# Performance work log

Hardware: AMD Instinct MI355X
Metric: run time of the kernel (lower is better)

Reference implementation:

```python
import jax, jax.numpy as jnp
import numpy as np

C_S, C_Z, N_HEADS = 768, 64, 12
HEAD_DIM = C_S // N_HEADS
L = 1024
EPS = 1e-5


def _ln(x, g, b):
    mu = jnp.mean(x, axis=-1, keepdims=True)
    var = jnp.mean((x - mu) ** 2, axis=-1, keepdims=True)
    return (x - mu) * jax.lax.rsqrt(var + EPS) * g + b


def setup_inputs() -> dict:
    key = jax.random.key(0)
    ks = jax.random.split(key, 12)
    w = lambda k, shp, fan_in: jax.random.normal(k, shp, dtype=jnp.float32) / np.sqrt(fan_in)
    return {
        "single": jax.random.normal(ks[0], (L, C_S), dtype=jnp.float32),
        "pair": jax.random.normal(ks[1], (L, L, C_Z), dtype=jnp.float32),
        "ln_s_g": jnp.ones((C_S,), jnp.float32),
        "ln_s_b": jnp.zeros((C_S,), jnp.float32),
        "ln_z_g": jnp.ones((C_Z,), jnp.float32),
        "ln_z_b": jnp.zeros((C_Z,), jnp.float32),
        "Wq": w(ks[2], (C_S, C_S), C_S),
        "Wk": w(ks[3], (C_S, C_S), C_S),
        "Wv": w(ks[4], (C_S, C_S), C_S),
        "Wb": w(ks[5], (C_Z, N_HEADS), C_Z),
        "Wout": w(ks[6], (C_S, C_S), C_S),
        "bout": jnp.zeros((C_S,), jnp.float32),
        "Wgate": w(ks[7], (C_S, C_S), C_S),
        "bgate": jnp.zeros((C_S,), jnp.float32),
    }


def reference(single, pair, ln_s_g, ln_s_b, ln_z_g, ln_z_b,
              Wq, Wk, Wv, Wb, Wout, bout, Wgate, bgate):
    Lq = single.shape[0]
    s = _ln(single, ln_s_g, ln_s_b)                    # [L, C_S]
    z = _ln(pair, ln_z_g, ln_z_b)                      # [L, L, C_Z]
    q = (s @ Wq).reshape(Lq, N_HEADS, HEAD_DIM)
    k = (s @ Wk).reshape(Lq, N_HEADS, HEAD_DIM)
    v = (s @ Wv).reshape(Lq, N_HEADS, HEAD_DIM)
    logits = jnp.einsum('ihd,jhd->hij', q, k) / np.sqrt(HEAD_DIM)
    logits = logits + jnp.einsum('ijc,ch->hij', z, Wb)  # pair bias per head
    attn = jax.nn.softmax(logits, axis=-1)              # [H, L, L]
    out = jnp.einsum('hij,jhd->ihd', attn, v).reshape(Lq, C_S)
    return single + jax.nn.sigmoid(s @ Wgate + bgate) * (out @ Wout + bout)
```

## Files before the change

kernel.cpp:

```cpp
#include <hip/hip_runtime.h>

#define LQ 1024
#define CS 768
#define CZ 64
#define NH 12
#define HD 64

typedef float4 f4;
using bf16x8 = __attribute__((ext_vector_type(8))) short;
using f32x4  = __attribute__((ext_vector_type(4))) float;

static __device__ __forceinline__ unsigned short f2bf(float f) {
  unsigned int u = __float_as_uint(f);
  u += 0x7fffu + ((u >> 16) & 1u);
  return (unsigned short)(u >> 16);
}
static __device__ __forceinline__ float bf2f(unsigned short b) {
  return __uint_as_float(((unsigned int)b) << 16);
}
static __device__ __forceinline__ unsigned cvtpk(float lo, float hi) {
  unsigned r;
  asm("v_cvt_pk_bf16_f32 %0, %1, %2" : "=v"(r) : "v"(lo), "v"(hi));
  return r;
}

__global__ __launch_bounds__(256) void ln_wconv_k(
    const float* __restrict__ x, const float* __restrict__ g,
    const float* __restrict__ b, unsigned short* __restrict__ s_out,
    const float* __restrict__ Wq, const float* __restrict__ Wk,
    const float* __restrict__ Wv, const float* __restrict__ Wg,
    const float* __restrict__ Wo, unsigned short* __restrict__ wt) {
  const int bid = blockIdx.x;
  const int t = threadIdx.x;
  if (bid < LQ) {
    const int row = bid;
    const float* xr = x + (size_t)row * CS;
    float v0 = xr[t], v1 = xr[t + 256], v2 = xr[t + 512];
    float s1 = v0 + v1 + v2;
    float s2 = v0 * v0 + v1 * v1 + v2 * v2;
#pragma unroll
    for (int m = 1; m < 64; m <<= 1) {
      s1 += __shfl_xor(s1, m);
      s2 += __shfl_xor(s2, m);
    }
    __shared__ float r1[4], r2[4];
    const int wid = t >> 6;
    if ((t & 63) == 0) { r1[wid] = s1; r2[wid] = s2; }
    __syncthreads();
    s1 = r1[0] + r1[1] + r1[2] + r1[3];
    s2 = r2[0] + r2[1] + r2[2] + r2[3];
    const float mu = s1 * (1.f / CS);
    const float var = s2 * (1.f / CS) - mu * mu;
    const float rs = rsqrtf(var + 1e-5f);
    s_out[(size_t)row * CS + t]       = f2bf((v0 - mu) * rs * g[t]       + b[t]);
    s_out[(size_t)row * CS + t + 256] = f2bf((v1 - mu) * rs * g[t + 256] + b[t + 256]);
    s_out[(size_t)row * CS + t + 512] = f2bf((v2 - mu) * rs * g[t + 512] + b[t + 512]);
  } else {
    int r = bid - LQ;
    const int bz = r / 144; r %= 144;
    const int n0 = (r % 12) * 64, k0 = (r / 12) * 64;
    const float* W;
    switch (bz) {
      case 0: W = Wq; break;
      case 1: W = Wk; break;
      case 2: W = Wv; break;
      case 3: W = Wg; break;
      default: W = Wo; break;
    }
    unsigned short* o = wt + (size_t)bz * CS * CS;
    __shared__ float T[64][68];
    {
      const int rr = t >> 4, c = (t & 15) * 4;
#pragma unroll
      for (int u = 0; u < 4; ++u) {
        const f4 v = *(const f4*)&W[(size_t)(k0 + rr + u * 16) * CS + n0 + c];
        *(f4*)&T[rr + u * 16][c] = v;
      }
    }
    __syncthreads();
    {
      const int rn = t >> 2, ck = (t & 3) * 16;
      __align__(16) unsigned short tmp[16];
#pragma unroll
      for (int u = 0; u < 16; ++u) tmp[u] = f2bf(T[ck + u][rn]);
      unsigned short* dst = &o[(size_t)(n0 + rn) * CS + k0 + ck];
      *(uint4*)dst = ((const uint4*)tmp)[0];
      *(uint4*)(dst + 8) = ((const uint4*)tmp)[1];
    }
  }
}

__global__ __launch_bounds__(256) void pair_k(
    const float* __restrict__ pair, const float* __restrict__ zg,
    const float* __restrict__ zb, const float* __restrict__ Wb,
    unsigned short* __restrict__ biasF) {
  __shared__ __align__(16) unsigned short zs[256 * 64];
  __shared__ float rstats[256], mstats[256];
  const int t = threadIdx.x;
  const int w = t >> 6, lane = t & 63, g = lane >> 4, c = lane & 15;
  const int bid = blockIdx.x;
  const int i0 = (bid >> 4) * 4;
  const int j0 = (bid & 15) * 64;

  const f32x4* src = (const f32x4*)(pair + ((size_t)(i0 + w) * LQ + j0) * CZ);
  f32x4 vv[16];
#pragma unroll
  for (int u = 0; u < 16; ++u) vv[u] = src[u * 64 + lane];

  const int csafe = (c < NH) ? c : 0;
  float C1 = 0.f, C2 = 0.f;
  for (int ch = 0; ch < CZ; ++ch) {
    const float wv = (c < NH) ? Wb[ch * NH + csafe] : 0.f;
    C1 = fmaf(zg[ch], wv, C1);
    C2 = fmaf(zb[ch], wv, C2);
  }
  bf16x8 wf0, wf1;
#pragma unroll
  for (int u = 0; u < 8; ++u) {
    const float w0 = (c < NH) ? zg[g * 8 + u] * Wb[(g * 8 + u) * NH + csafe] : 0.f;
    const float w1 = (c < NH) ? zg[32 + g * 8 + u] * Wb[(32 + g * 8 + u) * NH + csafe] : 0.f;
    wf0[u] = (short)f2bf(w0);
    wf1[u] = (short)f2bf(w1);
  }

#pragma unroll
  for (int u = 0; u < 16; ++u) {
    const int idx = u * 64 + lane;
    const int j = idx >> 4;
    const int kq = idx & 15;
    const int row = w * 64 + j;
    const int chunk = kq >> 1, half = kq & 1;
    uint2 pk;
    pk.x = cvtpk(vv[u][0], vv[u][1]);
    pk.y = cvtpk(vv[u][2], vv[u][3]);
    *(uint2*)&zs[row * 64 + ((chunk ^ (row & 7)) << 3) + (half << 2)] = pk;
  }
  __syncthreads();

  {
    float s1 = 0.f, s2 = 0.f;
    const int r7 = t & 7;
#pragma unroll
    for (int k = 0; k < 8; ++k) {
      const uint4 q = *(const uint4*)&zs[t * 64 + ((k ^ r7) << 3)];
      const float f0 = __uint_as_float(q.x << 16), f1 = __uint_as_float(q.x & 0xffff0000u);
      const float f2 = __uint_as_float(q.y << 16), f3 = __uint_as_float(q.y & 0xffff0000u);
      const float f4v = __uint_as_float(q.z << 16), f5 = __uint_as_float(q.z & 0xffff0000u);
      const float f6 = __uint_as_float(q.w << 16), f7 = __uint_as_float(q.w & 0xffff0000u);
      s1 += ((f0 + f1) + (f2 + f3)) + ((f4v + f5) + (f6 + f7));
      s2 += ((f0 * f0 + f1 * f1) + (f2 * f2 + f3 * f3))
          + ((f4v * f4v + f5 * f5) + (f6 * f6 + f7 * f7));
    }
    const float mu = s1 * (1.f / CZ);
    const float var = s2 * (1.f / CZ) - mu * mu;
    const float rs = rsqrtf(var + 1e-5f);
    rstats[t] = rs;
    mstats[t] = -rs * mu;
  }
  __syncthreads();

  const int il = c & 3, jl = c >> 2;
  const int gi = i0 >> 4, ga = (i0 >> 2) & 3;
  const size_t hd_base = ((size_t)gi * 16) * 4 * 256 + (size_t)ga * 64;
#pragma unroll
  for (int mm = 0; mm < 4; ++mm) {
    const int jloc = w * 16 + mm * 4;
    const int arow = il * 64 + jloc + jl;
    const int r7a = arow & 7;
    const bf16x8 a0 = *(const bf16x8*)&zs[arow * 64 + ((g ^ r7a) << 3)];
    const bf16x8 a1 = *(const bf16x8*)&zs[arow * 64 + (((4 + g) ^ r7a) << 3)];
    f32x4 dd = (f32x4){0.f, 0.f, 0.f, 0.f};
    dd = __builtin_amdgcn_mfma_f32_16x16x32_bf16(a0, wf0, dd, 0, 0, 0);
    dd = __builtin_amdgcn_mfma_f32_16x16x32_bf16(a1, wf1, dd, 0, 0, 0);

    const int jg = jloc + g;
    const float rs0 = rstats[jg],       mp0 = mstats[jg];
    const float rs1 = rstats[64 + jg],  mp1 = mstats[64 + jg];
    const float rs2 = rstats[128 + jg], mp2 = mstats[128 + jg];
    const float rs3 = rstats[192 + jg], mp3 = mstats[192 + jg];
    if (c < NH) {
      const float b0 = fmaf(rs0, dd[0], fmaf(mp0, C1, C2));
      const float b1 = fmaf(rs1, dd[1], fmaf(mp1, C1, C2));
      const float b2 = fmaf(rs2, dd[2], fmaf(mp2, C1, C2));
      const float b3 = fmaf(rs3, dd[3], fmaf(mp3, C1, C2));
      const int jj = j0 + jg;
      const size_t base = ((size_t)c * 64) * 16384 + hd_base
                        + (size_t)(jj >> 6) * 1024
                        + (size_t)((jj >> 4) & 3) * 256
                        + (jj & 15) * 4;
      uint2 st;
      st.x = cvtpk(b0, b1);
      st.y = cvtpk(b2, b3);
      *(uint2*)&biasF[base] = st;
    }
  }
}

__global__ __launch_bounds__(256) void gemm_qkvg_k(
    const unsigned short* __restrict__ s, const unsigned short* __restrict__ wt,
    const float* __restrict__ bg,
    unsigned short* __restrict__ qb, unsigned short* __restrict__ kb,
    unsigned short* __restrict__ vt, float* __restrict__ gpre) {
  __shared__ __align__(16) unsigned short As[64][88];
  __shared__ __align__(16) unsigned short Bs[128][88];
  const int t = threadIdx.x;
  const int w = t >> 6, lane = t & 63, g = lane >> 4, c = lane & 15;
  const int wm = w >> 1, wn = w & 1;
  const int bx = blockIdx.x % 24, by = blockIdx.x / 24;
  const int m0 = by * 64;
  const int wid = bx / 6;
  const int nl0 = (bx % 6) * 128;
  const unsigned short* B = wt + (size_t)wid * CS * CS;

  f32x4 acc[2][4];
#pragma unroll
  for (int i = 0; i < 2; ++i)
#pragma unroll
    for (int j = 0; j < 4; ++j) acc[i][j] = (f32x4){0.f, 0.f, 0.f, 0.f};

  const int sra = t >> 2, sha = (t & 3) * 16;
  const int srb = t >> 1, shb = (t & 1) * 32;
  for (int kt = 0; kt < CS; kt += 64) {
    __syncthreads();
#pragma unroll
    for (int u = 0; u < 2; ++u)
      *(uint4*)&As[sra][sha + u * 8] = *(const uint4*)&s[(size_t)(m0 + sra) * CS + kt + sha + u * 8];
#pragma unroll
    for (int u = 0; u < 4; ++u)
      *(uint4*)&Bs[srb][shb + u * 8] = *(const uint4*)&B[(size_t)(nl0 + srb) * CS + kt + shb + u * 8];
    __syncthreads();
#pragma unroll
    for (int kk = 0; kk < 64; kk += 32) {
      bf16x8 af[2], bfr[4];
#pragma unroll
      for (int i = 0; i < 2; ++i) af[i] = *(const bf16x8*)&As[wm * 32 + i * 16 + c][kk + g * 8];
#pragma unroll
      for (int j = 0; j < 4; ++j) bfr[j] = *(const bf16x8*)&Bs[wn * 64 + j * 16 + c][kk + g * 8];
#pragma unroll
      for (int i = 0; i < 2; ++i)
#pragma unroll
        for (int j = 0; j < 4; ++j)
          acc[i][j] = __builtin_amdgcn_mfma_f32_16x16x32_bf16(af[i], bfr[j], acc[i][j], 0, 0, 0);
    }
  }
#pragma unroll
  for (int i = 0; i < 2; ++i) {
#pragma unroll
    for (int j = 0; j < 4; ++j) {
      const int mb = m0 + wm * 32 + i * 16 + g * 4;
      const int nn = nl0 + wn * 64 + j * 16 + c;
      const f32x4 a = acc[i][j];
      if (wid == 0) {
#pragma unroll
        for (int r = 0; r < 4; ++r) qb[(size_t)(mb + r) * CS + nn] = f2bf(a[r] * 0.125f);
      } else if (wid == 1) {
#pragma unroll
        for (int r = 0; r < 4; ++r) kb[(size_t)(mb + r) * CS + nn] = f2bf(a[r]);
      } else if (wid == 2) {
        ushort4 pk;
        pk.x = f2bf(a[0]); pk.y = f2bf(a[1]); pk.z = f2bf(a[2]); pk.w = f2bf(a[3]);
        *(ushort4*)&vt[(size_t)nn * LQ + mb] = pk;
      } else {
        const float bb = bg[nn];
#pragma unroll
        for (int r = 0; r < 4; ++r) gpre[(size_t)(mb + r) * CS + nn] = a[r] + bb;
      }
    }
  }
}

__global__ __launch_bounds__(256) void attn_k(
    const unsigned short* __restrict__ q, const unsigned short* __restrict__ k,
    const unsigned short* __restrict__ vt, const unsigned short* __restrict__ biasF,
    float* __restrict__ Opart, float* __restrict__ ml) {
  __shared__ __align__(16) unsigned short Qs[64][88];
  __shared__ __align__(16) unsigned short Ks[2][64][88];
  __shared__ __align__(16) unsigned short Vts[2][64][88];
  __shared__ __align__(16) unsigned short Ps[4][16][88];
  const int bx = blockIdx.x, h = blockIdx.y, z = blockIdx.z;
  const int i0 = bx * 64;
  const int jb = z * 512;
  const int t = threadIdx.x;
  const int w = t >> 6, lane = t & 63, g = lane >> 4, c = lane & 15;
  const int sr = t >> 2, sc = (t & 3) * 16;

#pragma unroll
  for (int u = 0; u < 2; ++u) {
    *(uint4*)&Qs[sr][sc + u * 8]     = *(const uint4*)&q[(size_t)(i0 + sr) * CS + h * HD + sc + u * 8];
    *(uint4*)&Ks[0][sr][sc + u * 8]  = *(const uint4*)&k[(size_t)(jb + sr) * CS + h * HD + sc + u * 8];
    *(uint4*)&Vts[0][sr][sc + u * 8] = *(const uint4*)&vt[(size_t)(h * HD + sr) * LQ + jb + sc + u * 8];
  }
  const size_t bbase = ((((size_t)h * 64 + (bx * 4 + w)) * 16 + (size_t)z * 8) * 4) * 256 + lane * 4;
  ushort4 bcur[4];
#pragma unroll
  for (int nb = 0; nb < 4; ++nb) bcur[nb] = *(const ushort4*)&biasF[bbase + nb * 256];
  __syncthreads();

  const bf16x8 aq0 = *(const bf16x8*)&Qs[w * 16 + c][g * 8];
  const bf16x8 aq1 = *(const bf16x8*)&Qs[w * 16 + c][32 + g * 8];

  f32x4 acc_o[4];
#pragma unroll
  for (int nb = 0; nb < 4; ++nb) acc_o[nb] = (f32x4){0.f, 0.f, 0.f, 0.f};
  float m_run[4] = {-1e30f, -1e30f, -1e30f, -1e30f};
  float l_run[4] = {0.f, 0.f, 0.f, 0.f};

  for (int jt = 0; jt < 8; ++jt) {
    const int cur = jt & 1;
    uint4 kr0, kr1, vr0, vr1;
    ushort4 bnx[4];
    if (jt < 7) {
      const int jn = jb + (jt + 1) * 64;
      kr0 = *(const uint4*)&k[(size_t)(jn + sr) * CS + h * HD + sc];
      kr1 = *(const uint4*)&k[(size_t)(jn + sr) * CS + h * HD + sc + 8];
      vr0 = *(const uint4*)&vt[(size_t)(h * HD + sr) * LQ + jn + sc];
      vr1 = *(const uint4*)&vt[(size_t)(h * HD + sr) * LQ + jn + sc + 8];
#pragma unroll
      for (int nb = 0; nb < 4; ++nb)
        bnx[nb] = *(const ushort4*)&biasF[bbase + (size_t)(jt + 1) * 1024 + nb * 256];
    }

    f32x4 sa[4];
#pragma unroll
    for (int nb = 0; nb < 4; ++nb) {
      f32x4 ci;
      ci[0] = bf2f(bcur[nb].x); ci[1] = bf2f(bcur[nb].y);
      ci[2] = bf2f(bcur[nb].z); ci[3] = bf2f(bcur[nb].w);
      const bf16x8 b0 = *(const bf16x8*)&Ks[cur][nb * 16 + c][g * 8];
      const bf16x8 b1 = *(const bf16x8*)&Ks[cur][nb * 16 + c][32 + g * 8];
      ci = __builtin_amdgcn_mfma_f32_16x16x32_bf16(aq0, b0, ci, 0, 0, 0);
      ci = __builtin_amdgcn_mfma_f32_16x16x32_bf16(aq1, b1, ci, 0, 0, 0);
      sa[nb] = ci;
    }

    float mt[4];
#pragma unroll
    for (int r = 0; r < 4; ++r) {
      float v = fmaxf(fmaxf(sa[0][r], sa[1][r]), fmaxf(sa[2][r], sa[3][r]));
      v = fmaxf(v, __shfl_xor(v, 1));
      v = fmaxf(v, __shfl_xor(v, 2));
      v = fmaxf(v, __shfl_xor(v, 4));
      v = fmaxf(v, __shfl_xor(v, 8));
      mt[r] = v;
    }
    float scale[4], ps[4];
#pragma unroll
    for (int r = 0; r < 4; ++r) {
      const float mn = fmaxf(m_run[r], mt[r]);
      scale[r] = __expf(m_run[r] - mn);
      m_run[r] = mn;
      ps[r] = 0.f;
    }
#pragma unroll
    for (int nb = 0; nb < 4; ++nb) {
#pragma unroll
      for (int r = 0; r < 4; ++r) {
        const float p = __expf(sa[nb][r] - m_run[r]);
        ps[r] += p;
        Ps[w][g * 4 + r][nb * 16 + c] = f2bf(p);
      }
    }
#pragma unroll
    for (int r = 0; r < 4; ++r) {
      float v = ps[r];
      v += __shfl_xor(v, 1);
      v += __shfl_xor(v, 2);
      v += __shfl_xor(v, 4);
      v += __shfl_xor(v, 8);
      l_run[r] = l_run[r] * scale[r] + v;
#pragma unroll
      for (int nb = 0; nb < 4; ++nb) acc_o[nb][r] *= scale[r];
    }

#pragma unroll
    for (int kb = 0; kb < 2; ++kb) {
      const bf16x8 pa = *(const bf16x8*)&Ps[w][c][kb * 32 + g * 8];
#pragma unroll
      for (int nb = 0; nb < 4; ++nb) {
        const bf16x8 bv = *(const bf16x8*)&Vts[cur][nb * 16 + c][kb * 32 + g * 8];
        acc_o[nb] = __builtin_amdgcn_mfma_f32_16x16x32_bf16(pa, bv, acc_o[nb], 0, 0, 0);
      }
    }

    if (jt < 7) {
      *(uint4*)&Ks[cur ^ 1][sr][sc]      = kr0;
      *(uint4*)&Ks[cur ^ 1][sr][sc + 8]  = kr1;
      *(uint4*)&Vts[cur ^ 1][sr][sc]     = vr0;
      *(uint4*)&Vts[cur ^ 1][sr][sc + 8] = vr1;
      __syncthreads();
#pragma unroll
      for (int nb = 0; nb < 4; ++nb) bcur[nb] = bnx[nb];
    }
  }

  const size_t rowb = (size_t)(z * NH + h) * LQ + i0 + w * 16 + g * 4;
#pragma unroll
  for (int nb = 0; nb < 4; ++nb)
#pragma unroll
    for (int r = 0; r < 4; ++r)
      Opart[(rowb + r) * HD + nb * 16 + c] = acc_o[nb][r];
  if (c == 0) {
#pragma unroll
    for (int r = 0; r < 4; ++r) {
      ml[(rowb + r) * 2]     = m_run[r];
      ml[(rowb + r) * 2 + 1] = l_run[r];
    }
  }
}

__global__ __launch_bounds__(256) void combine_k(
    const float* __restrict__ Opart, const float* __restrict__ ml,
    unsigned short* __restrict__ attno) {
  const int t = threadIdx.x;
  const int row = blockIdx.x * 4 + (t >> 6);
  const int d = t & 63;
  const int h = row >> 10, i = row & 1023;
  const size_t r0 = (size_t)h * LQ + i;
  const size_t r1 = (size_t)(NH + h) * LQ + i;
  const float m0 = ml[r0 * 2], l0 = ml[r0 * 2 + 1];
  const float m1 = ml[r1 * 2], l1 = ml[r1 * 2 + 1];
  const float M = fmaxf(m0, m1);
  const float a0 = __expf(m0 - M), a1 = __expf(m1 - M);
  const float L = a0 * l0 + a1 * l1;
  const float o = (a0 * Opart[r0 * HD + d] + a1 * Opart[r1 * HD + d]) / L;
  attno[(size_t)i * CS + h * HD + d] = f2bf(o);
}

__global__ __launch_bounds__(256) void gemm_final_k(
    const unsigned short* __restrict__ A, const unsigned short* __restrict__ wt,
    const float* __restrict__ bout, const float* __restrict__ single,
    const float* __restrict__ gpre, float* __restrict__ out) {
  __shared__ __align__(16) unsigned short As[64][88];
  __shared__ __align__(16) unsigned short Bs[128][88];
  const int t = threadIdx.x;
  const int wave = t >> 6, lane = t & 63, g = lane >> 4, c = lane & 15;
  const int wm = wave >> 1, wn = wave & 1;
  const int m0 = blockIdx.y * 64;
  const int nl0 = blockIdx.x * 128;
  const unsigned short* B = wt + (size_t)4 * CS * CS;

  f32x4 acc[2][4];
#pragma unroll
  for (int i = 0; i < 2; ++i)
#pragma unroll
    for (int j = 0; j < 4; ++j) acc[i][j] = (f32x4){0.f, 0.f, 0.f, 0.f};

  const int sra = t >> 2, sha = (t & 3) * 16;
  const int srb = t >> 1, shb = (t & 1) * 32;
  for (int kt = 0; kt < CS; kt += 64) {
    __syncthreads();
#pragma unroll
    for (int u = 0; u < 2; ++u)
      *(uint4*)&As[sra][sha + u * 8] = *(const uint4*)&A[(size_t)(m0 + sra) * CS + kt + sha + u * 8];
#pragma unroll
    for (int u = 0; u < 4; ++u)
      *(uint4*)&Bs[srb][shb + u * 8] = *(const uint4*)&B[(size_t)(nl0 + srb) * CS + kt + shb + u * 8];
    __syncthreads();
#pragma unroll
    for (int kk = 0; kk < 64; kk += 32) {
      bf16x8 af[2], bfr[4];
#pragma unroll
      for (int i = 0; i < 2; ++i) af[i] = *(const bf16x8*)&As[wm * 32 + i * 16 + c][kk + g * 8];
#pragma unroll
      for (int j = 0; j < 4; ++j) bfr[j] = *(const bf16x8*)&Bs[wn * 64 + j * 16 + c][kk + g * 8];
#pragma unroll
      for (int i = 0; i < 2; ++i)
#pragma unroll
        for (int j = 0; j < 4; ++j)
          acc[i][j] = __builtin_amdgcn_mfma_f32_16x16x32_bf16(af[i], bfr[j], acc[i][j], 0, 0, 0);
    }
  }

#pragma unroll
  for (int i = 0; i < 2; ++i) {
#pragma unroll
    for (int j = 0; j < 4; ++j) {
      const int mb = m0 + wm * 32 + i * 16 + g * 4;
      const int nn = nl0 + wn * 64 + j * 16 + c;
      const float bb = bout[nn];
      const f32x4 a = acc[i][j];
#pragma unroll
      for (int r = 0; r < 4; ++r) {
        const size_t idx = (size_t)(mb + r) * CS + nn;
        const float gate = 1.f / (1.f + __expf(-gpre[idx]));
        out[idx] = single[idx] + gate * (a[r] + bb);
      }
    }
  }
}

extern "C" void kernel_launch(void* const* d_in, const int* in_sizes, int n_in,
                              void* d_out, int out_size, void* d_ws, size_t ws_size,
                              hipStream_t stream) {
  const float* single = (const float*)d_in[0];
  const float* pair   = (const float*)d_in[1];
  const float* ln_s_g = (const float*)d_in[2];
  const float* ln_s_b = (const float*)d_in[3];
  const float* ln_z_g = (const float*)d_in[4];
  const float* ln_z_b = (const float*)d_in[5];
  const float* Wq     = (const float*)d_in[6];
  const float* Wk     = (const float*)d_in[7];
  const float* Wv     = (const float*)d_in[8];
  const float* Wb     = (const float*)d_in[9];
  const float* Wout   = (const float*)d_in[10];
  const float* bout   = (const float*)d_in[11];
  const float* Wgate  = (const float*)d_in[12];
  const float* bgate  = (const float*)d_in[13];
  float* out = (float*)d_out;

  unsigned short* s_bf  = (unsigned short*)d_ws;
  unsigned short* wt    = s_bf  + (size_t)LQ * CS;
  unsigned short* q_bf  = wt    + (size_t)5 * CS * CS;
  unsigned short* k_bf  = q_bf  + (size_t)LQ * CS;
  unsigned short* vt_bf = k_bf  + (size_t)LQ * CS;
  unsigned short* attno = vt_bf + (size_t)CS * LQ;
  unsigned short* biasF = attno + (size_t)LQ * CS;
  float* gpre  = (float*)(biasF + (size_t)NH * LQ * LQ);
  float* Opart = gpre  + (size_t)LQ * CS;
  float* mlw   = Opart + (size_t)2 * NH * LQ * HD;

  hipLaunchKernelGGL(pair_k, dim3(4096), dim3(256), 0, stream,
                     pair, ln_z_g, ln_z_b, Wb, biasF);
  hipLaunchKernelGGL(ln_wconv_k, dim3(LQ + 720), dim3(256), 0, stream,
                     single, ln_s_g, ln_s_b, s_bf, Wq, Wk, Wv, Wgate, Wout, wt);
  hipLaunchKernelGGL(gemm_qkvg_k, dim3(384), dim3(256), 0, stream,
                     s_bf, wt, bgate, q_bf, k_bf, vt_bf, gpre);
  hipLaunchKernelGGL(attn_k, dim3(16, NH, 2), dim3(256), 0, stream,
                     q_bf, k_bf, vt_bf, biasF, Opart, mlw);
  hipLaunchKernelGGL(combine_k, dim3(3072), dim3(256), 0, stream,
                     Opart, mlw, attno);
  hipLaunchKernelGGL(gemm_final_k, dim3(6, 16), dim3(256), 0, stream,
                     attno, wt, bout, single, gpre, out);
}
```

Before: 130.1 us.

## Merge pair-bias and QKVG GEMM into one launch; stage bias stores through LDS

Merges the pair layernorm/bias kernel and the QKVG projection GEMM into a single launch, with block index choosing the role, so the small GEMM can overlap with the bandwidth-heavy pair pass and one launch disappears. The bias output is now staged in shared memory and written with 16-byte coalesced stores instead of scattered 8-byte stores. The trade-off is that the shared-memory footprint becomes the union of both roles (about 41 KB), which can reduce occupancy for the pair blocks, and the GEMM blocks are scheduled after the 4096 pair blocks.

```diff
diff --git a/kernel.cpp b/kernel.cpp
--- a/kernel.cpp
+++ b/kernel.cpp
@@ -90,180 +90,193 @@
   }
 }
 
-__global__ __launch_bounds__(256) void pair_k(
+__global__ __launch_bounds__(256) void qkvg_pair_k(
+    const unsigned short* __restrict__ s, const unsigned short* __restrict__ wt,
+    const float* __restrict__ bg,
+    unsigned short* __restrict__ qb, unsigned short* __restrict__ kb,
+    unsigned short* __restrict__ vt, float* __restrict__ gpre,
     const float* __restrict__ pair, const float* __restrict__ zg,
     const float* __restrict__ zb, const float* __restrict__ Wb,
     unsigned short* __restrict__ biasF) {
-  __shared__ __align__(16) unsigned short zs[256 * 64];
-  __shared__ float rstats[256], mstats[256];
+  __shared__ __align__(16) unsigned char smraw[41152];
   const int t = threadIdx.x;
   const int w = t >> 6, lane = t & 63, g = lane >> 4, c = lane & 15;
-  const int bid = blockIdx.x;
-  const int i0 = (bid >> 4) * 4;
-  const int j0 = (bid & 15) * 64;
-
-  const f32x4* src = (const f32x4*)(pair + ((size_t)(i0 + w) * LQ + j0) * CZ);
-  f32x4 vv[16];
-#pragma unroll
-  for (int u = 0; u < 16; ++u) vv[u] = src[u * 64 + lane];
-
-  const int csafe = (c < NH) ? c : 0;
-  float C1 = 0.f, C2 = 0.f;
-  for (int ch = 0; ch < CZ; ++ch) {
-    const float wv = (c < NH) ? Wb[ch * NH + csafe] : 0.f;
-    C1 = fmaf(zg[ch], wv, C1);
-    C2 = fmaf(zb[ch], wv, C2);
-  }
-  bf16x8 wf0, wf1;
-#pragma unroll
-  for (int u = 0; u < 8; ++u) {
-    const float w0 = (c < NH) ? zg[g * 8 + u] * Wb[(g * 8 + u) * NH + csafe] : 0.f;
-    const float w1 = (c < NH) ? zg[32 + g * 8 + u] * Wb[(32 + g * 8 + u) * NH + csafe] : 0.f;
-    wf0[u] = (short)f2bf(w0);
-    wf1[u] = (short)f2bf(w1);
-  }
-
-#pragma unroll
-  for (int u = 0; u < 16; ++u) {
-    const int idx = u * 64 + lane;
-    const int j = idx >> 4;
-    const int kq = idx & 15;
-    const int row = w * 64 + j;
-    const int chunk = kq >> 1, half = kq & 1;
-    uint2 pk;
-    pk.x = cvtpk(vv[u][0], vv[u][1]);
-    pk.y = cvtpk(vv[u][2], vv[u][3]);
-    *(uint2*)&zs[row * 64 + ((chunk ^ (row & 7)) << 3) + (half << 2)] = pk;
-  }
-  __syncthreads();
-
-  {
-    float s1 = 0.f, s2 = 0.f;
-    const int r7 = t & 7;
-#pragma unroll
-    for (int k = 0; k < 8; ++k) {
-      const uint4 q = *(const uint4*)&zs[t * 64 + ((k ^ r7) << 3)];
-      const float f0 = __uint_as_float(q.x << 16), f1 = __uint_as_float(q.x & 0xffff0000u);
-      const float f2 = __uint_as_float(q.y << 16), f3 = __uint_as_float(q.y & 0xffff0000u);
-      const float f4v = __uint_as_float(q.z << 16), f5 = __uint_as_float(q.z & 0xffff0000u);
-      const float f6 = __uint_as_float(q.w << 16), f7 = __uint_as_float(q.w & 0xffff0000u);
-      s1 += ((f0 + f1) + (f2 + f3)) + ((f4v + f5) + (f6 + f7));
-      s2 += ((f0 * f0 + f1 * f1) + (f2 * f2 + f3 * f3))
-          + ((f4v * f4v + f5 * f5) + (f6 * f6 + f7 * f7));
-    }
-    const float mu = s1 * (1.f / CZ);
-    const float var = s2 * (1.f / CZ) - mu * mu;
-    const float rs = rsqrtf(var + 1e-5f);
-    rstats[t] = rs;
-    mstats[t] = -rs * mu;
-  }
-  __syncthreads();
-
-  const int il = c & 3, jl = c >> 2;
-  const int gi = i0 >> 4, ga = (i0 >> 2) & 3;
-  const size_t hd_base = ((size_t)gi * 16) * 4 * 256 + (size_t)ga * 64;
-#pragma unroll
-  for (int mm = 0; mm < 4; ++mm) {
-    const int jloc = w * 16 + mm * 4;
-    const int arow = il * 64 + jloc + jl;
-    const int r7a = arow & 7;
-    const bf16x8 a0 = *(const bf16x8*)&zs[arow * 64 + ((g ^ r7a) << 3)];
-    const bf16x8 a1 = *(const bf16x8*)&zs[arow * 64 + (((4 + g) ^ r7a) << 3)];
-    f32x4 dd = (f32x4){0.f, 0.f, 0.f, 0.f};
-    dd = __builtin_amdgcn_mfma_f32_16x16x32_bf16(a0, wf0, dd, 0, 0, 0);
-    dd = __builtin_amdgcn_mfma_f32_16x16x32_bf16(a1, wf1, dd, 0, 0, 0);
-
-    const int jg = jloc + g;
-    const float rs0 = rstats[jg],       mp0 = mstats[jg];
-    const float rs1 = rstats[64 + jg],  mp1 = mstats[64 + jg];
-    const float rs2 = rstats[128 + jg], mp2 = mstats[128 + jg];
-    const float rs3 = rstats[192 + jg], mp3 = mstats[192 + jg];
-    if (c < NH) {
-      const float b0 = fmaf(rs0, dd[0], fmaf(mp0, C1, C2));
-      const float b1 = fmaf(rs1, dd[1], fmaf(mp1, C1, C2));
-      const float b2 = fmaf(rs2, dd[2], fmaf(mp2, C1, C2));
-      const float b3 = fmaf(rs3, dd[3], fmaf(mp3, C1, C2));
-      const int jj = j0 + jg;
-      const size_t base = ((size_t)c * 64) * 16384 + hd_base
-                        + (size_t)(jj >> 6) * 1024
-                        + (size_t)((jj >> 4) & 3) * 256
-                        + (jj & 15) * 4;
-      uint2 st;
-      st.x = cvtpk(b0, b1);
-      st.y = cvtpk(b2, b3);
-      *(uint2*)&biasF[base] = st;
-    }
-  }
-}
-
-__global__ __launch_bounds__(256) void gemm_qkvg_k(
-    const unsigned short* __restrict__ s, const unsigned short* __restrict__ wt,
-    const float* __restrict__ bg,
-    unsigned short* __restrict__ qb, unsigned short* __restrict__ kb,
-    unsigned short* __restrict__ vt, float* __restrict__ gpre) {
-  __shared__ __align__(16) unsigned short As[64][88];
-  __shared__ __align__(16) unsigned short Bs[128][88];
-  const int t = threadIdx.x;
-  const int w = t >> 6, lane = t & 63, g = lane >> 4, c = lane & 15;
-  const int wm = w >> 1, wn = w & 1;
-  const int bx = blockIdx.x % 24, by = blockIdx.x / 24;
-  const int m0 = by * 64;
-  const int wid = bx / 6;
-  const int nl0 = (bx % 6) * 128;
-  const unsigned short* B = wt + (size_t)wid * CS * CS;
-
-  f32x4 acc[2][4];
-#pragma unroll
-  for (int i = 0; i < 2; ++i)
-#pragma unroll
-    for (int j = 0; j < 4; ++j) acc[i][j] = (f32x4){0.f, 0.f, 0.f, 0.f};
-
-  const int sra = t >> 2, sha = (t & 3) * 16;
-  const int srb = t >> 1, shb = (t & 1) * 32;
-  for (int kt = 0; kt < CS; kt += 64) {
-    __syncthreads();
-#pragma unroll
-    for (int u = 0; u < 2; ++u)
-      *(uint4*)&As[sra][sha + u * 8] = *(const uint4*)&s[(size_t)(m0 + sra) * CS + kt + sha + u * 8];
-#pragma unroll
-    for (int u = 0; u < 4; ++u)
-      *(uint4*)&Bs[srb][shb + u * 8] = *(const uint4*)&B[(size_t)(nl0 + srb) * CS + kt + shb + u * 8];
-    __syncthreads();
-#pragma unroll
-    for (int kk = 0; kk < 64; kk += 32) {
-      bf16x8 af[2], bfr[4];
-#pragma unroll
-      for (int i = 0; i < 2; ++i) af[i] = *(const bf16x8*)&As[wm * 32 + i * 16 + c][kk + g * 8];
-#pragma unroll
-      for (int j = 0; j < 4; ++j) bfr[j] = *(const bf16x8*)&Bs[wn * 64 + j * 16 + c][kk + g * 8];
-#pragma unroll
-      for (int i = 0; i < 2; ++i)
-#pragma unroll
-        for (int j = 0; j < 4; ++j)
-          acc[i][j] = __builtin_amdgcn_mfma_f32_16x16x32_bf16(af[i], bfr[j], acc[i][j], 0, 0, 0);
-    }
-  }
-#pragma unroll
-  for (int i = 0; i < 2; ++i) {
-#pragma unroll
-    for (int j = 0; j < 4; ++j) {
-      const int mb = m0 + wm * 32 + i * 16 + g * 4;
-      const int nn = nl0 + wn * 64 + j * 16 + c;
-      const f32x4 a = acc[i][j];
-      if (wid == 0) {
-#pragma unroll
-        for (int r = 0; r < 4; ++r) qb[(size_t)(mb + r) * CS + nn] = f2bf(a[r] * 0.125f);
-      } else if (wid == 1) {
-#pragma unroll
-        for (int r = 0; r < 4; ++r) kb[(size_t)(mb + r) * CS + nn] = f2bf(a[r]);
-      } else if (wid == 2) {
-        ushort4 pk;
-        pk.x = f2bf(a[0]); pk.y = f2bf(a[1]); pk.z = f2bf(a[2]); pk.w = f2bf(a[3]);
-        *(ushort4*)&vt[(size_t)nn * LQ + mb] = pk;
-      } else {
-        const float bb = bg[nn];
-#pragma unroll
-        for (int r = 0; r < 4; ++r) gpre[(size_t)(mb + r) * CS + nn] = a[r] + bb;
+
+  if (blockIdx.x < 4096) {
+    unsigned short* zs = (unsigned short*)smraw;
+    unsigned short* outT = (unsigned short*)(smraw + 32768);
+    float* rstats = (float*)(smraw + 39104);
+    float* mstats = (float*)(smraw + 40128);
+    const int bid = blockIdx.x;
+    const int i0 = (bid >> 4) * 4;
+    const int j0 = (bid & 15) * 64;
+
+    const f32x4* src = (const f32x4*)(pair + ((size_t)(i0 + w) * LQ + j0) * CZ);
+    f32x4 vv[16];
+#pragma unroll
+    for (int u = 0; u < 16; ++u) vv[u] = src[u * 64 + lane];
+
+    const int csafe = (c < NH) ? c : 0;
+    float C1 = 0.f, C2 = 0.f;
+    for (int ch = 0; ch < CZ; ++ch) {
+      const float wv = (c < NH) ? Wb[ch * NH + csafe] : 0.f;
+      C1 = fmaf(zg[ch], wv, C1);
+      C2 = fmaf(zb[ch], wv, C2);
+    }
+    bf16x8 wf0, wf1;
+#pragma unroll
+    for (int u = 0; u < 8; ++u) {
+      const float w0 = (c < NH) ? zg[g * 8 + u] * Wb[(g * 8 + u) * NH + csafe] : 0.f;
+      const float w1 = (c < NH) ? zg[32 + g * 8 + u] * Wb[(32 + g * 8 + u) * NH + csafe] : 0.f;
+      wf0[u] = (short)f2bf(w0);
+      wf1[u] = (short)f2bf(w1);
+    }
+
+#pragma unroll
+    for (int u = 0; u < 16; ++u) {
+      const int idx = u * 64 + lane;
+      const int j = idx >> 4;
+      const int kq = idx & 15;
+      const int row = w * 64 + j;
+      const int chunk = kq >> 1, half = kq & 1;
+      uint2 pk;
+      pk.x = cvtpk(vv[u][0], vv[u][1]);
+      pk.y = cvtpk(vv[u][2], vv[u][3]);
+      *(uint2*)&zs[row * 64 + ((chunk ^ (row & 7)) << 3) + (half << 2)] = pk;
+    }
+    __syncthreads();
+
+    {
+      float s1 = 0.f, s2 = 0.f;
+      const int r7 = t & 7;
+#pragma unroll
+      for (int k = 0; k < 8; ++k) {
+        const uint4 q = *(const uint4*)&zs[t * 64 + ((k ^ r7) << 3)];
+        const float f0 = __uint_as_float(q.x << 16), f1 = __uint_as_float(q.x & 0xffff0000u);
+        const float f2 = __uint_as_float(q.y << 16), f3 = __uint_as_float(q.y & 0xffff0000u);
+        const float f4v = __uint_as_float(q.z << 16), f5 = __uint_as_float(q.z & 0xffff0000u);
+        const float f6 = __uint_as_float(q.w << 16), f7 = __uint_as_float(q.w & 0xffff0000u);
+        s1 += ((f0 + f1) + (f2 + f3)) + ((f4v + f5) + (f6 + f7));
+        s2 += ((f0 * f0 + f1 * f1) + (f2 * f2 + f3 * f3))
+            + ((f4v * f4v + f5 * f5) + (f6 * f6 + f7 * f7));
+      }
+      const float mu = s1 * (1.f / CZ);
+      const float var = s2 * (1.f / CZ) - mu * mu;
+      const float rs = rsqrtf(var + 1e-5f);
+      rstats[t] = rs;
+      mstats[t] = -rs * mu;
+    }
+    __syncthreads();
+
+    const int il = c & 3, jl = c >> 2;
+#pragma unroll
+    for (int mm = 0; mm < 4; ++mm) {
+      const int jloc = w * 16 + mm * 4;
+      const int arow = il * 64 + jloc + jl;
+      const int r7a = arow & 7;
+      const bf16x8 a0 = *(const bf16x8*)&zs[arow * 64 + ((g ^ r7a) << 3)];
+      const bf16x8 a1 = *(const bf16x8*)&zs[arow * 64 + (((4 + g) ^ r7a) << 3)];
+      f32x4 dd = (f32x4){0.f, 0.f, 0.f, 0.f};
+      dd = __builtin_amdgcn_mfma_f32_16x16x32_bf16(a0, wf0, dd, 0, 0, 0);
+      dd = __builtin_amdgcn_mfma_f32_16x16x32_bf16(a1, wf1, dd, 0, 0, 0);
+
+      const int jg = jloc + g;
+      const float rs0 = rstats[jg],       mp0 = mstats[jg];
+      const float rs1 = rstats[64 + jg],  mp1 = mstats[64 + jg];
+      const float rs2 = rstats[128 + jg], mp2 = mstats[128 + jg];
+      const float rs3 = rstats[192 + jg], mp3 = mstats[192 + jg];
+      if (c < NH) {
+        const float b0 = fmaf(rs0, dd[0], fmaf(mp0, C1, C2));
+        const float b1 = fmaf(rs1, dd[1], fmaf(mp1, C1, C2));
+        const float b2 = fmaf(rs2, dd[2], fmaf(mp2, C1, C2));
+        const float b3 = fmaf(rs3, dd[3], fmaf(mp3, C1, C2));
+        uint2 st;
+        st.x = cvtpk(b0, b1);
+        st.y = cvtpk(b2, b3);
+        *(uint2*)&outT[c * 264 + (jg >> 4) * 64 + (jg & 15) * 4] = st;
+      }
+    }
+    __syncthreads();
+
+    const int gi = i0 >> 4, ga = (i0 >> 2) & 3;
+    const int jt0 = j0 >> 6;
+#pragma unroll
+    for (int rep = 0; rep < 2; ++rep) {
+      const int idx = rep * 256 + t;
+      if (idx < 384) {
+        const int hh = idx >> 5;
+        const int sp = (idx >> 3) & 3;
+        const int sub = idx & 7;
+        const uint4 v = *(const uint4*)&outT[hh * 264 + sp * 64 + sub * 8];
+        const size_t flat = ((((size_t)hh * 64 + gi) * 16 + jt0) * 4 + sp) * 256
+                          + (size_t)ga * 64 + sub * 8;
+        *(uint4*)&biasF[flat] = v;
+      }
+    }
+  } else {
+    unsigned short (*As)[88] = (unsigned short (*)[88])smraw;
+    unsigned short (*Bs)[88] = (unsigned short (*)[88])(smraw + 64 * 88 * 2);
+    const int gb = blockIdx.x - 4096;
+    const int wm = w >> 1, wn = w & 1;
+    const int bx = gb % 24, by = gb / 24;
+    const int m0 = by * 64;
+    const int wid = bx / 6;
+    const int nl0 = (bx % 6) * 128;
+    const unsigned short* B = wt + (size_t)wid * CS * CS;
+
+    f32x4 acc[2][4];
+#pragma unroll
+    for (int i = 0; i < 2; ++i)
+#pragma unroll
+      for (int j = 0; j < 4; ++j) acc[i][j] = (f32x4){0.f, 0.f, 0.f, 0.f};
+
+    const int sra = t >> 2, sha = (t & 3) * 16;
+    const int srb = t >> 1, shb = (t & 1) * 32;
+    for (int kt = 0; kt < CS; kt += 64) {
+      __syncthreads();
+#pragma unroll
+      for (int u = 0; u < 2; ++u)
+        *(uint4*)&As[sra][sha + u * 8] = *(const uint4*)&s[(size_t)(m0 + sra) * CS + kt + sha + u * 8];
+#pragma unroll
+      for (int u = 0; u < 4; ++u)
+        *(uint4*)&Bs[srb][shb + u * 8] = *(const uint4*)&B[(size_t)(nl0 + srb) * CS + kt + shb + u * 8];
+      __syncthreads();
+#pragma unroll
+      for (int kk = 0; kk < 64; kk += 32) {
+        bf16x8 af[2], bfr[4];
+#pragma unroll
+        for (int i = 0; i < 2; ++i) af[i] = *(const bf16x8*)&As[wm * 32 + i * 16 + c][kk + g * 8];
+#pragma unroll
+        for (int j = 0; j < 4; ++j) bfr[j] = *(const bf16x8*)&Bs[wn * 64 + j * 16 + c][kk + g * 8];
+#pragma unroll
+        for (int i = 0; i < 2; ++i)
+#pragma unroll
+          for (int j = 0; j < 4; ++j)
+            acc[i][j] = __builtin_amdgcn_mfma_f32_16x16x32_bf16(af[i], bfr[j], acc[i][j], 0, 0, 0);
+      }
+    }
+#pragma unroll
+    for (int i = 0; i < 2; ++i) {
+#pragma unroll
+      for (int j = 0; j < 4; ++j) {
+        const int mb = m0 + wm * 32 + i * 16 + g * 4;
+        const int nn = nl0 + wn * 64 + j * 16 + c;
+        const f32x4 a = acc[i][j];
+        if (wid == 0) {
+#pragma unroll
+          for (int r = 0; r < 4; ++r) qb[(size_t)(mb + r) * CS + nn] = f2bf(a[r] * 0.125f);
+        } else if (wid == 1) {
+#pragma unroll
+          for (int r = 0; r < 4; ++r) kb[(size_t)(mb + r) * CS + nn] = f2bf(a[r]);
+        } else if (wid == 2) {
+          ushort4 pk;
+          pk.x = f2bf(a[0]); pk.y = f2bf(a[1]); pk.z = f2bf(a[2]); pk.w = f2bf(a[3]);
+          *(ushort4*)&vt[(size_t)nn * LQ + mb] = pk;
+        } else {
+          const float bb = bg[nn];
+#pragma unroll
+          for (int r = 0; r < 4; ++r) gpre[(size_t)(mb + r) * CS + nn] = a[r] + bb;
+        }
       }
     }
   }
@@ -519,12 +532,11 @@
   float* Opart = gpre  + (size_t)LQ * CS;
   float* mlw   = Opart + (size_t)2 * NH * LQ * HD;
 
-  hipLaunchKernelGGL(pair_k, dim3(4096), dim3(256), 0, stream,
-                     pair, ln_z_g, ln_z_b, Wb, biasF);
   hipLaunchKernelGGL(ln_wconv_k, dim3(LQ + 720), dim3(256), 0, stream,
                      single, ln_s_g, ln_s_b, s_bf, Wq, Wk, Wv, Wgate, Wout, wt);
-  hipLaunchKernelGGL(gemm_qkvg_k, dim3(384), dim3(256), 0, stream,
-                     s_bf, wt, bgate, q_bf, k_bf, vt_bf, gpre);
+  hipLaunchKernelGGL(qkvg_pair_k, dim3(4096 + 384), dim3(256), 0, stream,
+                     s_bf, wt, bgate, q_bf, k_bf, vt_bf, gpre,
+                     pair, ln_z_g, ln_z_b, Wb, biasF);
   hipLaunchKernelGGL(attn_k, dim3(16, NH, 2), dim3(256), 0, stream,
                      q_bf, k_bf, vt_bf, biasF, Opart, mlw);
   hipLaunchKernelGGL(combine_k, dim3(3072), dim3(256), 0, stream,
```

Result: slower. 148.1 us (+13.9%).
